# Kernel optimization log

Measured on AMD Instinct MI355X. Metric: run time of the kernel, lower is better.

The kernel has to match this reference:

```python
import jax, jax.numpy as jnp
import numpy as np


def _conv2d_valid(x, w):
    # x: (N, C, H, W), w: (O, C, kH, kW) -> (N, O, H-kH+1, W-kW+1)
    return jax.lax.conv_general_dilated(
        x, w, window_strides=(1, 1), padding='VALID',
        dimension_numbers=('NCHW', 'OIHW', 'NCHW'))


def setup_inputs() -> dict:
    key = jax.random.key(0)
    kx, ky = jax.random.split(key)
    x = jax.random.normal(kx, (16, 64, 128, 128), dtype=jnp.float32)
    y = jax.random.normal(ky, (64, 64, 16, 16), dtype=jnp.float32)
    return {"x": x, "y": y}


def reference(x, y):
    # Normalize each of the K kernels to unit L2 norm (sum over C, kH, kW).
    normed_y = y / jnp.sqrt(jnp.sum(y * y, axis=(1, 2, 3), keepdims=True))
    # Per-window L2 norm of x via ones-kernel box conv over x^2.
    ones_kernel = jnp.ones(y.shape, dtype=x.dtype)
    x_norm = jnp.sqrt(_conv2d_valid(x * x, ones_kernel))
    # Normalized cross-correlation, clamped at zero.
    diss = _conv2d_valid(x, normed_y) / x_norm
    return jax.nn.relu(diss)
```

## Files before the change

### kernel.cpp

```cpp
#include <hip/hip_runtime.h>
#include <stdint.h>

#define GAS __attribute__((address_space(1)))
#define LAS __attribute__((address_space(3)))

typedef __attribute__((ext_vector_type(8))) short short8;
typedef __attribute__((ext_vector_type(4))) float float4v;
typedef __attribute__((ext_vector_type(4))) unsigned int uint4v;

__device__ __forceinline__ unsigned short f2bf(float f) {
  union { float f; unsigned int u; } v; v.f = f;
  unsigned int r = v.u + 0x7fffu + ((v.u >> 16) & 1u);
  return (unsigned short)(r >> 16);
}

__device__ __forceinline__ void async_g2l16(const void* g, void* l) {
  __builtin_amdgcn_global_load_lds((const GAS unsigned int*)g,
                                   (LAS unsigned int*)l, 16, 0, 0);
}

__device__ __forceinline__ void vmem_drain() {
  asm volatile("s_waitcnt vmcnt(0)" ::: "memory");
}

__global__ void knorm_y(const float* __restrict__ y, unsigned short* __restrict__ y_t2) {
  int o = blockIdx.x;
  int tid = threadIdx.x;
  const float* yo = y + o * 16384;
  float s = 0.f;
  for (int idx = tid; idx < 16384; idx += 256) { float v = yo[idx]; s += v * v; }
  for (int off = 32; off; off >>= 1) s += __shfl_down(s, off, 64);
  __shared__ float red[4];
  if ((tid & 63) == 0) red[tid >> 6] = s;
  __syncthreads();
  float rn = 1.0f / sqrtf(red[0] + red[1] + red[2] + red[3]);
  int og = o >> 4, ol = o & 15;
  for (int idx = tid; idx < 16384; idx += 256) {
    int c = idx >> 8, dy = (idx >> 4) & 15, dx = idx & 15;
    int t = dy * 16 + dx;
    int cb = c >> 5, q = (c >> 3) & 3, j = c & 7;
    size_t dst = (size_t)t * 4096 + (size_t)(og * 2 + cb) * 512 + (q * 16 + ol) * 8 + j;
    y_t2[dst] = f2bf(yo[idx] * rn);
  }
}

__global__ void ktrans_x(const float* __restrict__ x, unsigned short* __restrict__ x_t,
                         float* __restrict__ s) {
  int h = blockIdx.x, n = blockIdx.y;
  int tid = threadIdx.x;
  __shared__ __align__(16) unsigned short tb[8192];
  __shared__ float sb[256];
  const float* xb = x + ((size_t)n * 64) * 16384 + h * 128;
  int w = tid & 127, half = tid >> 7;
  float acc = 0.f;
#pragma unroll
  for (int cs = 0; cs < 4; ++cs) {
    short8 tmp;
#pragma unroll
    for (int j = 0; j < 8; ++j) {
      int c = half * 32 + cs * 8 + j;
      float v = xb[(size_t)c * 16384 + w];
      tmp[j] = (short)f2bf(v);
      acc += v * v;
    }
    int chunk = (half * 4 + cs) ^ (w & 7);
    *(short8*)(tb + w * 64 + chunk * 8) = tmp;
  }
  sb[tid] = acc;
  __syncthreads();
  uint4v* dst = (uint4v*)(x_t + ((size_t)(n * 128 + h)) * 8192);
  const uint4v* src = (const uint4v*)tb;
  for (int idx = tid; idx < 1024; idx += 256) dst[idx] = src[idx];
  if (tid < 128) s[((size_t)(n * 128 + h)) * 128 + tid] = sb[tid] + sb[tid + 128];
}

__global__ void knorm_x(const float* __restrict__ s, float* __restrict__ invn) {
  int i = blockIdx.x, n = blockIdx.y;
  int tid = threadIdx.x;
  __shared__ float colsum[128];
  const float* sp = s + ((size_t)(n * 128 + i)) * 128;
  float a = 0.f;
#pragma unroll
  for (int dy = 0; dy < 16; ++dy) a += sp[dy * 128 + tid];
  colsum[tid] = a;
  __syncthreads();
  if (tid < 113) {
    float acc = 0.f;
#pragma unroll
    for (int dx = 0; dx < 16; ++dx) acc += colsum[tid + dx];
    invn[((size_t)n * 113 + i) * 113 + tid] = 1.0f / sqrtf(acc);
  }
}

__launch_bounds__(256, 4)
__global__ void kconv(const unsigned short* __restrict__ x_t,
                      const unsigned short* __restrict__ y_t2,
                      const float* __restrict__ invn,
                      float* __restrict__ out) {
  int lin = blockIdx.y * 113 + blockIdx.x;
  int wg = (lin & 7) * 226 + (lin >> 3);
  int i = wg % 113;
  int n = wg / 113;
  int tid = threadIdx.x;
  int lane = tid & 63, wave = tid >> 6;
  int lane15 = lane & 15, q = lane >> 4;
  int wrow = wave >> 1, wcol = wave & 1;

  __shared__ __align__(16) char smem[32768];
  char* const A0 = smem;
  char* const A1 = smem + 16384;

  const char* xrow0 = (const char*)(x_t + ((size_t)(n * 128 + i)) * 8192);

  auto stageA = [&](int dy, char* buf) {
    const char* src = xrow0 + (size_t)dy * 16384;
#pragma unroll
    for (int it = 0; it < 4; ++it) {
      int chunk = it * 256 + wave * 64;
      async_g2l16(src + (chunk + lane) * 16, buf + chunk * 16);
    }
  };

  const short8* ybase = (const short8*)(y_t2 + (size_t)wcol * 2048 + (size_t)lane * 8);
  auto loadB = [&](int t, short8 bf[2][2]) {
    const short8* p = ybase + (size_t)t * 512;
    bf[0][0] = p[0];
    bf[0][1] = p[64];
    bf[1][0] = p[128];
    bf[1][1] = p[192];
  };

  float4v acc[4][2];
#pragma unroll
  for (int mt = 0; mt < 4; ++mt)
#pragma unroll
    for (int nt = 0; nt < 2; ++nt) acc[mt][nt] = (float4v){0.f, 0.f, 0.f, 0.f};

  int abase[4];
#pragma unroll
  for (int mt = 0; mt < 4; ++mt) abase[mt] = (wrow * 64 + mt * 16 + lane15) * 128;

  short8 b0[2][2], b1[2][2];
  stageA(0, A0);
  loadB(0, b0);
  vmem_drain();
  __syncthreads();

#pragma unroll 1
  for (int dy = 0; dy < 16; ++dy) {
    char* Ab = (dy & 1) ? A1 : A0;
    if (dy < 15) {
      __builtin_amdgcn_sched_barrier(0);
      stageA(dy + 1, (dy & 1) ? A0 : A1);
      __builtin_amdgcn_sched_barrier(0);
    }
#pragma unroll
    for (int dx = 0; dx < 16; ++dx) {
      int t = dy * 16 + dx;
      short8(&bc)[2][2] = (dx & 1) ? b1 : b0;
      short8(&bn)[2][2] = (dx & 1) ? b0 : b1;
      if (t < 255) loadB(t + 1, bn);
      int xr = (lane15 + dx) & 7;
#pragma unroll
      for (int cb = 0; cb < 2; ++cb) {
        int aoff = dx * 128 + (((q + cb * 4) ^ xr) << 4);
#pragma unroll
        for (int mt = 0; mt < 4; ++mt) {
          short8 a = *(const short8*)(Ab + abase[mt] + aoff);
          acc[mt][0] = __builtin_amdgcn_mfma_f32_16x16x32_bf16(a, bc[0][cb], acc[mt][0], 0, 0, 0);
          acc[mt][1] = __builtin_amdgcn_mfma_f32_16x16x32_bf16(a, bc[1][cb], acc[mt][1], 0, 0, 0);
        }
      }
    }
    asm volatile("s_waitcnt vmcnt(4)" ::: "memory");
    __syncthreads();
  }

  float* cs = (float*)smem;
  float* ivs = cs + 4352;
  const float* ivp = invn + ((size_t)n * 113 + i) * 113;
  if (tid < 128) ivs[tid] = (tid < 113) ? ivp[tid] : 0.f;
  float* op = out + (size_t)n * 64 * 12769 + (size_t)i * 113;
#pragma unroll 1
  for (int p = 0; p < 2; ++p) {
    if (wcol == p) {
#pragma unroll
      for (int mt = 0; mt < 4; ++mt)
#pragma unroll
        for (int nt = 0; nt < 2; ++nt) {
          int row = nt * 16 + lane15;
          int j0 = wrow * 64 + mt * 16 + q * 4;
          *(float4v*)(cs + row * 132 + j0) = acc[mt][nt];
        }
    }
    __syncthreads();
    for (int idx = tid; idx < 4096; idx += 256) {
      int o2 = idx >> 7, j = idx & 127;
      if (j < 113) {
        float v = cs[o2 * 132 + j] * ivs[j];
        op[(size_t)(p * 32 + o2) * 12769 + j] = fmaxf(v, 0.f);
      }
    }
    __syncthreads();
  }
}

extern "C" void kernel_launch(void* const* d_in, const int* in_sizes, int n_in,
                              void* d_out, int out_size, void* d_ws, size_t ws_size,
                              hipStream_t stream) {
  const float* x = (const float*)d_in[0];
  const float* y = (const float*)d_in[1];
  float* out = (float*)d_out;
  char* ws = (char*)d_ws;
  unsigned short* x_t = (unsigned short*)ws;
  unsigned short* y_t2 = (unsigned short*)(ws + 33554432);
  float* s = (float*)(ws + 35651584);
  float* invn = (float*)(ws + 36700160);

  hipLaunchKernelGGL(knorm_y, dim3(64), dim3(256), 0, stream, y, y_t2);
  hipLaunchKernelGGL(ktrans_x, dim3(128, 16), dim3(256), 0, stream, x, x_t, s);
  hipLaunchKernelGGL(knorm_x, dim3(113, 16), dim3(128), 0, stream, s, invn);
  hipLaunchKernelGGL(kconv, dim3(113, 16), dim3(256), 0, stream, x_t, y_t2, invn, out);
}
```

Before: 525.6 us.

## Switch conv GEMM to 32x32x16 MFMA and store epilogue directly from registers

The main conv kernel now uses 32x32x16 bf16 MFMA tiles instead of 16x16x32. This needs a re-laid-out normalized-weight buffer and a new LDS read pattern with the same swizzle, and it aims to cut LDS A-operand reads per FLOP and the number of MFMA issues. The epilogue drops the LDS staging pass and its barriers. Each lane now applies inv-norm and ReLU and writes float4 runs straight to global memory, which trades coalescing for fewer syncs. Launch bounds drop to 3 blocks per SIMD to allow more registers.

```diff
diff --git a/kernel.cpp b/kernel.cpp
--- a/kernel.cpp
+++ b/kernel.cpp
@@ -6,6 +6,7 @@
 
 typedef __attribute__((ext_vector_type(8))) short short8;
 typedef __attribute__((ext_vector_type(4))) float float4v;
+typedef __attribute__((ext_vector_type(16))) float float16v;
 typedef __attribute__((ext_vector_type(4))) unsigned int uint4v;
 
 __device__ __forceinline__ unsigned short f2bf(float f) {
@@ -34,12 +35,12 @@
   if ((tid & 63) == 0) red[tid >> 6] = s;
   __syncthreads();
   float rn = 1.0f / sqrtf(red[0] + red[1] + red[2] + red[3]);
-  int og = o >> 4, ol = o & 15;
+  int og = o >> 5, ol = o & 31;
   for (int idx = tid; idx < 16384; idx += 256) {
     int c = idx >> 8, dy = (idx >> 4) & 15, dx = idx & 15;
     int t = dy * 16 + dx;
-    int cb = c >> 5, q = (c >> 3) & 3, j = c & 7;
-    size_t dst = (size_t)t * 4096 + (size_t)(og * 2 + cb) * 512 + (q * 16 + ol) * 8 + j;
+    int kc = c >> 4, half = (c >> 3) & 1, j = c & 7;
+    size_t dst = (size_t)t * 4096 + (size_t)(og * 4 + kc) * 512 + (half * 32 + ol) * 8 + j;
     y_t2[dst] = f2bf(yo[idx] * rn);
   }
 }
@@ -92,7 +93,7 @@
   }
 }
 
-__launch_bounds__(256, 4)
+__launch_bounds__(256, 3)
 __global__ void kconv(const unsigned short* __restrict__ x_t,
                       const unsigned short* __restrict__ y_t2,
                       const float* __restrict__ invn,
@@ -103,7 +104,7 @@
   int n = wg / 113;
   int tid = threadIdx.x;
   int lane = tid & 63, wave = tid >> 6;
-  int lane15 = lane & 15, q = lane >> 4;
+  int lane31 = lane & 31, l5 = lane >> 5;
   int wrow = wave >> 1, wcol = wave & 1;
 
   __shared__ __align__(16) char smem[32768];
@@ -121,26 +122,25 @@
     }
   };
 
-  const short8* ybase = (const short8*)(y_t2 + (size_t)wcol * 2048 + (size_t)lane * 8);
-  auto loadB = [&](int t, short8 bf[2][2]) {
+  const short8* ybase = (const short8*)y_t2 + (size_t)wcol * 256 + lane;
+  auto loadB = [&](int t, short8 bf[4]) {
     const short8* p = ybase + (size_t)t * 512;
-    bf[0][0] = p[0];
-    bf[0][1] = p[64];
-    bf[1][0] = p[128];
-    bf[1][1] = p[192];
+    bf[0] = p[0];
+    bf[1] = p[64];
+    bf[2] = p[128];
+    bf[3] = p[192];
   };
 
-  float4v acc[4][2];
-#pragma unroll
-  for (int mt = 0; mt < 4; ++mt)
-#pragma unroll
-    for (int nt = 0; nt < 2; ++nt) acc[mt][nt] = (float4v){0.f, 0.f, 0.f, 0.f};
-
-  int abase[4];
-#pragma unroll
-  for (int mt = 0; mt < 4; ++mt) abase[mt] = (wrow * 64 + mt * 16 + lane15) * 128;
-
-  short8 b0[2][2], b1[2][2];
+  float16v acc[2];
+  acc[0] = 0.f;
+  acc[1] = 0.f;
+
+  int abase[2];
+#pragma unroll
+  for (int mt = 0; mt < 2; ++mt)
+    abase[mt] = (wrow * 64 + mt * 32 + lane31) * 128;
+
+  short8 b0[4], b1[4];
   stageA(0, A0);
   loadB(0, b0);
   vmem_drain();
@@ -157,18 +157,17 @@
 #pragma unroll
     for (int dx = 0; dx < 16; ++dx) {
       int t = dy * 16 + dx;
-      short8(&bc)[2][2] = (dx & 1) ? b1 : b0;
-      short8(&bn)[2][2] = (dx & 1) ? b0 : b1;
+      short8(&bc)[4] = (dx & 1) ? b1 : b0;
+      short8(&bn)[4] = (dx & 1) ? b0 : b1;
       if (t < 255) loadB(t + 1, bn);
-      int xr = (lane15 + dx) & 7;
-#pragma unroll
-      for (int cb = 0; cb < 2; ++cb) {
-        int aoff = dx * 128 + (((q + cb * 4) ^ xr) << 4);
-#pragma unroll
-        for (int mt = 0; mt < 4; ++mt) {
+      int xr = (lane31 + dx) & 7;
+#pragma unroll
+      for (int kc = 0; kc < 4; ++kc) {
+#pragma unroll
+        for (int mt = 0; mt < 2; ++mt) {
+          int aoff = dx * 128 + (((kc * 2 + l5) ^ xr) << 4);
           short8 a = *(const short8*)(Ab + abase[mt] + aoff);
-          acc[mt][0] = __builtin_amdgcn_mfma_f32_16x16x32_bf16(a, bc[0][cb], acc[mt][0], 0, 0, 0);
-          acc[mt][1] = __builtin_amdgcn_mfma_f32_16x16x32_bf16(a, bc[1][cb], acc[mt][1], 0, 0, 0);
+          acc[mt] = __builtin_amdgcn_mfma_f32_32x32x16_bf16(a, bc[kc], acc[mt], 0, 0, 0);
         }
       }
     }
@@ -176,32 +175,26 @@
     __syncthreads();
   }
 
-  float* cs = (float*)smem;
-  float* ivs = cs + 4352;
   const float* ivp = invn + ((size_t)n * 113 + i) * 113;
-  if (tid < 128) ivs[tid] = (tid < 113) ? ivp[tid] : 0.f;
   float* op = out + (size_t)n * 64 * 12769 + (size_t)i * 113;
-#pragma unroll 1
-  for (int p = 0; p < 2; ++p) {
-    if (wcol == p) {
-#pragma unroll
-      for (int mt = 0; mt < 4; ++mt)
-#pragma unroll
-        for (int nt = 0; nt < 2; ++nt) {
-          int row = nt * 16 + lane15;
-          int j0 = wrow * 64 + mt * 16 + q * 4;
-          *(float4v*)(cs + row * 132 + j0) = acc[mt][nt];
-        }
-    }
-    __syncthreads();
-    for (int idx = tid; idx < 4096; idx += 256) {
-      int o2 = idx >> 7, j = idx & 127;
-      if (j < 113) {
-        float v = cs[o2 * 132 + j] * ivs[j];
-        op[(size_t)(p * 32 + o2) * 12769 + j] = fmaxf(v, 0.f);
+  int o = wcol * 32 + lane31;
+#pragma unroll
+  for (int mt = 0; mt < 2; ++mt) {
+#pragma unroll
+    for (int rg = 0; rg < 4; ++rg) {
+      int j0 = wrow * 64 + mt * 32 + rg * 8 + l5 * 4;
+      if (j0 <= 108) {
+        float4v iv = *(const float4v*)(ivp + j0);
+        float4v r;
+        r[0] = fmaxf(acc[mt][rg * 4 + 0] * iv[0], 0.f);
+        r[1] = fmaxf(acc[mt][rg * 4 + 1] * iv[1], 0.f);
+        r[2] = fmaxf(acc[mt][rg * 4 + 2] * iv[2], 0.f);
+        r[3] = fmaxf(acc[mt][rg * 4 + 3] * iv[3], 0.f);
+        *(float4v*)(op + (size_t)o * 12769 + j0) = r;
+      } else if (j0 == 112) {
+        op[(size_t)o * 12769 + 112] = fmaxf(acc[mt][rg * 4] * ivp[112], 0.f);
       }
     }
-    __syncthreads();
   }
 }
 
```

Result: slower. 606.1 us (+15.3%).
